# Performance work log

Hardware: AMD Instinct MI355X
Metric: run time of the kernel (lower is better)

## Reference

```python
import jax, jax.numpy as jnp
import numpy as np

B, S, H = 8, 8192, 128          # batch, num_cities, hidden_size
SSIZE, DSIZE = 2, 1             # static (x,y) feats, dynamic feats
STEPS = 20                      # station_num_lim (decode length)


def setup_inputs() -> dict:
    key = jax.random.key(0)
    ks = jax.random.split(key, 16)
    sc = 0.05
    inp = {
        'static': jax.random.normal(ks[0], (B, SSIZE, S), jnp.float32),
        'dynamic': jnp.zeros((B, DSIZE, S), jnp.float32),
        # Encoder convs (kernel_size=1 -> plain linear over channel dim)
        'W_s': jax.random.normal(ks[1], (H, SSIZE), jnp.float32) * sc,
        'b_s': jnp.zeros((H,), jnp.float32),
        'W_d': jax.random.normal(ks[2], (H, DSIZE), jnp.float32) * sc,
        'b_d': jnp.zeros((H,), jnp.float32),
        'W_dec': jax.random.normal(ks[3], (H, SSIZE), jnp.float32) * sc,
        'b_dec': jnp.zeros((H,), jnp.float32),
        # LSTMCell
        'W_ih': jax.random.normal(ks[4], (4 * H, H), jnp.float32) * sc,
        'W_hh': jax.random.normal(ks[5], (4 * H, H), jnp.float32) * sc,
        'b_ih': jnp.zeros((4 * H,), jnp.float32),
        'b_hh': jnp.zeros((4 * H,), jnp.float32),
        # Pointer projections
        'W_ref': jax.random.normal(ks[6], (H, H), jnp.float32) * sc,
        'b_ref': jnp.zeros((H,), jnp.float32),
        'W_pd': jax.random.normal(ks[7], (H, H), jnp.float32) * sc,
        'b_pd': jnp.zeros((H,), jnp.float32),
        'W_q': jax.random.normal(ks[8], (H, H), jnp.float32) * sc,
        'b_q': jnp.zeros((H,), jnp.float32),
        # Additive attention vector (Attention.W, shape (1,H) in torch)
        'W_att': jax.random.normal(ks[9], (H,), jnp.float32) * sc,
        'station_num_lim': STEPS,
    }
    return inp


def reference(static, dynamic, W_s, b_s, W_d, b_d, W_dec, b_dec,
              W_ih, W_hh, b_ih, b_hh, W_ref, b_ref, W_pd, b_pd,
              W_q, b_q, W_att, station_num_lim):
    Bb, _, Ss = static.shape
    Hh = W_s.shape[0]

    # static/dynamic encoders: Conv1d(k=1) == channelwise linear
    static_h = jnp.einsum('bis,hi->bhs', static, W_s) + b_s[None, :, None]
    dynamic_h = jnp.einsum('bis,hi->bhs', dynamic, W_d) + b_d[None, :, None]
    mask = jnp.ones((Bb, Ss), static.dtype)

    def lstm_cell(x, h, c):
        gates = x @ W_ih.T + b_ih + h @ W_hh.T + b_hh
        i, f, g, o = jnp.split(gates, 4, axis=1)
        c2 = jax.nn.sigmoid(f) * c + jax.nn.sigmoid(i) * jnp.tanh(g)
        h2 = jax.nn.sigmoid(o) * jnp.tanh(c2)
        return h2, c2

    def step(carry, _):
        dec_in, hh, cc = carry                      # dec_in: (B, SSIZE)
        dec_hidden = dec_in @ W_dec.T + b_dec       # decoder Encoder, (B, H)
        hh, cc = lstm_cell(dec_hidden, hh, cc)
        # per-step projections (as in the original Pointer.forward)
        ref = jnp.einsum('bhs,gh->bgs', static_h, W_ref) + b_ref[None, :, None]
        dyn = jnp.einsum('bhs,gh->bgs', dynamic_h, W_pd) + b_pd[None, :, None]
        q = hh @ W_q.T + b_q                        # (B, H)
        hidden = jnp.tanh(q[:, :, None] + ref + dyn)  # (B, H, S)
        attns = jnp.einsum('h,bhs->bs', W_att, hidden)
        probs = jax.nn.softmax(attns + mask * 10000.0, axis=1)
        prob = jnp.max(probs, axis=1)               # greedy (eval) select
        ptr = jnp.argmax(probs, axis=1)
        logp = jnp.log(prob)
        dec_in2 = jnp.take_along_axis(static, ptr[:, None, None], axis=2)[:, :, 0]
        return (dec_in2, hh, cc), (ptr, logp)

    dec0 = jnp.zeros((Bb, static.shape[1]), static.dtype)   # x0
    hh0 = jnp.zeros((Bb, Hh), static.dtype)
    cc0 = jnp.zeros((Bb, Hh), static.dtype)
    _, (tour_idx, tour_logp) = jax.lax.scan(
        step, (dec0, hh0, cc0), None, length=station_num_lim)
    return tour_idx.T, tour_logp.T                  # (B, steps), (B, steps)
```

## Files before the change

### kernel.cpp

```cpp
#include <hip/hip_runtime.h>
#include <hip/hip_bf16.h>


#define SS 8192
#define HH 128
#define NB 8

constexpr float kLog2e  = 1.4426950408889634f;
constexpr float kLn2    = 0.6931471805599453f;
constexpr float kBucket = 9.765625e-4f;
constexpr float kBL2e   = kLog2e * 9.765625e-4f;

__device__ __forceinline__ float fsig(float x) {
  return __builtin_amdgcn_rcpf(1.0f + __builtin_amdgcn_exp2f(-x * kLog2e));
}
__device__ __forceinline__ float ftanh(float x) {
  float z = __builtin_amdgcn_exp2f(x * (2.0f * kLog2e));
  return fmaf(-2.0f, __builtin_amdgcn_rcpf(z + 1.0f), 1.0f);
}

__device__ __forceinline__ unsigned long long cld64(const unsigned long long* p) {
  return __hip_atomic_load(p, __ATOMIC_RELAXED, __HIP_MEMORY_SCOPE_AGENT);
}
__device__ __forceinline__ void cst64(unsigned long long* p, unsigned long long v) {
  __hip_atomic_store(p, v, __ATOMIC_RELAXED, __HIP_MEMORY_SCOPE_AGENT);
}

__global__ __launch_bounds__(256, 1)
void drl4_kernel(const float* __restrict__ g_static,
                 const float* __restrict__ g_dynamic,
                 const float* __restrict__ W_s,  const float* __restrict__ b_s,
                 const float* __restrict__ W_d,  const float* __restrict__ b_d,
                 const float* __restrict__ W_dec,const float* __restrict__ b_dec,
                 const float* __restrict__ W_ih, const float* __restrict__ W_hh,
                 const float* __restrict__ b_ih, const float* __restrict__ b_hh,
                 const float* __restrict__ W_ref,const float* __restrict__ b_ref,
                 const float* __restrict__ W_pd, const float* __restrict__ b_pd,
                 const float* __restrict__ W_q,  const float* __restrict__ b_q,
                 const float* __restrict__ W_att,const int* __restrict__ steps_p,
                 float* __restrict__ out,
                 unsigned long long* __restrict__ krec,
                 unsigned long long* __restrict__ hhrec,
                 unsigned long long* __restrict__ frec) {
  const int tid = threadIdx.x;
  const int bid = blockIdx.x;
  const int b   = bid >> 5;
  const int blk = bid & 31;
  const int steps = *steps_p;

  __shared__ float4 s_pack[128];
  __shared__ float  s_ebias[128];
  __shared__ float  s_gb[512];
  __shared__ float  s_g1x[512];
  __shared__ float  s_g1y[512];
  __shared__ float  s_h[128];
  __shared__ __align__(16) float s_qe[128];
  __shared__ float  s_scr[256];

  const int city = blk * 256 + tid;
  const float sx = g_static[(b * 2 + 0) * SS + city];
  const float sy = g_static[(b * 2 + 1) * SS + city];
  const float dd = g_dynamic[b * SS + city];

  const int qrow  = (tid >> 6) * 32 + (tid & 31);
  const int qhalf = (tid >> 5) & 1;
  float wq[64];
  {
    const float* p = W_q + qrow * HH + qhalf * 64;
    #pragma unroll
    for (int j = 0; j < 64; j += 4) {
      float4 v = *(const float4*)(p + j);
      wq[j] = v.x; wq[j+1] = v.y; wq[j+2] = v.z; wq[j+3] = v.w;
    }
  }
  const int ho = tid & 15, hk = tid >> 4;
  float whh[8];
  {
    const float* p = W_hh + (blk * 16 + ho) * HH + hk * 8;
    #pragma unroll
    for (int j = 0; j < 8; j += 4) {
      float4 v = *(const float4*)(p + j);
      whh[j] = v.x; whh[j+1] = v.y; whh[j+2] = v.z; whh[j+3] = v.w;
    }
  }

  for (int g = tid; g < 512; g += 256) {
    const float* wr = W_ih + g * HH;
    float acc = b_ih[g] + b_hh[g];
    float ax = 0.f, ay = 0.f;
    for (int k = 0; k < HH; k += 4) {
      float4 w  = *(const float4*)(wr + k);
      float4 bd = *(const float4*)(b_dec + k);
      float4 d0 = *(const float4*)(W_dec + 2 * k);
      float4 d1 = *(const float4*)(W_dec + 2 * k + 4);
      acc = fmaf(w.x, bd.x, acc); ax = fmaf(w.x, d0.x, ax); ay = fmaf(w.x, d0.y, ay);
      acc = fmaf(w.y, bd.y, acc); ax = fmaf(w.y, d0.z, ax); ay = fmaf(w.y, d0.w, ay);
      acc = fmaf(w.z, bd.z, acc); ax = fmaf(w.z, d1.x, ax); ay = fmaf(w.z, d1.y, ay);
      acc = fmaf(w.w, bd.w, acc); ax = fmaf(w.w, d1.z, ax); ay = fmaf(w.w, d1.w, ay);
    }
    s_gb[g] = acc; s_g1x[g] = ax; s_g1y[g] = ay;
  }
  if (tid < 128) {
    float a0 = 0.f, a1 = 0.f, c0 = 0.f, e1 = 0.f, e2 = 0.f;
    const float* wr = W_ref + tid * HH;
    const float* wp = W_pd  + tid * HH;
    for (int k = 0; k < HH; k += 4) {
      float4 w  = *(const float4*)(wr + k);
      float4 v  = *(const float4*)(wp + k);
      float4 s0 = *(const float4*)(W_s + 2 * k);
      float4 s1 = *(const float4*)(W_s + 2 * k + 4);
      float4 bs = *(const float4*)(b_s + k);
      float4 wd = *(const float4*)(W_d + k);
      float4 bd = *(const float4*)(b_d + k);
      a0 = fmaf(w.x, s0.x, a0); a1 = fmaf(w.x, s0.y, a1); e1 = fmaf(w.x, bs.x, e1);
      c0 = fmaf(v.x, wd.x, c0); e2 = fmaf(v.x, bd.x, e2);
      a0 = fmaf(w.y, s0.z, a0); a1 = fmaf(w.y, s0.w, a1); e1 = fmaf(w.y, bs.y, e1);
      c0 = fmaf(v.y, wd.y, c0); e2 = fmaf(v.y, bd.y, e2);
      a0 = fmaf(w.z, s1.x, a0); a1 = fmaf(w.z, s1.y, a1); e1 = fmaf(w.z, bs.z, e1);
      c0 = fmaf(v.z, wd.z, c0); e2 = fmaf(v.z, bd.z, e2);
      a0 = fmaf(w.w, s1.z, a0); a1 = fmaf(w.w, s1.w, a1); e1 = fmaf(w.w, bs.w, e1);
      c0 = fmaf(v.w, wd.w, c0); e2 = fmaf(v.w, bd.w, e2);
    }
    const float sc = 2.0f * kLog2e;
    s_pack[tid]  = make_float4(a0 * sc, a1 * sc, c0 * sc, W_att[tid]);
    s_ebias[tid] = e1 + e2 + b_ref[tid] + b_pd[tid] + b_q[tid];
  }
  float cstate = 0.0f;
  __syncthreads();

  float zb[128], watt[128];
  #pragma unroll
  for (int h = 0; h < 128; ++h) {
    float4 p = s_pack[h];
    zb[h]   = __builtin_amdgcn_exp2f(fmaf(p.x, sx, fmaf(p.y, sy, p.z * dd)));
    watt[h] = p.w;
  }

  const int wv = tid >> 6;
  const int ln = tid & 63;
  for (int t = 0; t < steps; ++t) {
    float hp0 = 0.f, hp1 = 0.f, hp2 = 0.f, hp3 = 0.f;
    float selx = 0.f, sely = 0.f;
    if (t > 0) {
      if (tid < 128) {
        const unsigned expect = (unsigned)t;
        const unsigned long long* kp =
            krec + ((t - 1) & 1) * 1024 + b * 128;
        const unsigned long long* hp = hhrec + (t & 1) * 4096 + b * 512 + tid;
        unsigned long long k0, k1, h0, h1, h2, h3;
        for (;;) {
          k0 = cld64(kp + ln);       k1 = cld64(kp + 64 + ln);
          h0 = cld64(hp);            h1 = cld64(hp + 128);
          h2 = cld64(hp + 256);      h3 = cld64(hp + 384);
          if ((unsigned)(k0 >> 32) == expect && (unsigned)(k1 >> 32) == expect &&
              (unsigned)(h0 >> 32) == expect && (unsigned)(h1 >> 32) == expect &&
              (unsigned)(h2 >> 32) == expect && (unsigned)(h3 >> 32) == expect)
            break;
          __builtin_amdgcn_s_sleep(1);
        }
        unsigned u0 = (unsigned)k0, u1 = (unsigned)k1;
        unsigned wmax = u0 > u1 ? u0 : u1;
        #pragma unroll
        for (int k = 1; k < 64; k <<= 1) {
          unsigned o = __shfl_xor(wmax, k);
          wmax = wmax > o ? wmax : o;
        }
        const int ix = 8191 - (int)(wmax & 0x1FFFu);
        hp0 = __uint_as_float((unsigned)h0);
        hp1 = __uint_as_float((unsigned)h1);
        hp2 = __uint_as_float((unsigned)h2);
        hp3 = __uint_as_float((unsigned)h3);
        selx = g_static[(b * 2 + 0) * SS + ix];
        sely = g_static[(b * 2 + 1) * SS + ix];
      }
    }
    if (tid < 128) {
      float gi, gf, gg, go;
      if (t == 0) {
        gi = s_gb[tid];       gf = s_gb[tid + 128];
        gg = s_gb[tid + 256]; go = s_gb[tid + 384];
      } else {
        gi = fmaf(selx, s_g1x[tid],     fmaf(sely, s_g1y[tid],     s_gb[tid]     + hp0));
        gf = fmaf(selx, s_g1x[tid+128], fmaf(sely, s_g1y[tid+128], s_gb[tid+128] + hp1));
        gg = fmaf(selx, s_g1x[tid+256], fmaf(sely, s_g1y[tid+256], s_gb[tid+256] + hp2));
        go = fmaf(selx, s_g1x[tid+384], fmaf(sely, s_g1y[tid+384], s_gb[tid+384] + hp3));
      }
      cstate  = fmaf(fsig(gf), cstate, fsig(gi) * ftanh(gg));
      s_h[tid] = fsig(go) * ftanh(cstate);
    }
    __syncthreads();
    {
      const float* hs = s_h + (qhalf << 6);
      float qa = 0.f;
      #pragma unroll
      for (int u = 0; u < 64; ++u) qa = fmaf(wq[u], hs[u], qa);
      float qo = __shfl_xor(qa, 32);
      if (qhalf == 0) {
        float qe = (qa + qo + s_ebias[qrow]) * (2.0f * kLog2e);
        s_qe[qrow] = __builtin_amdgcn_exp2f(qe);
      }
    }
    {
      const float* hs2 = s_h + hk * 8;
      float pa = 0.f;
      #pragma unroll
      for (int u = 0; u < 8; ++u) pa = fmaf(whh[u], hs2[u], pa);
      s_scr[tid] = pa;
    }
    __syncthreads();
    if (tid < 16) {
      float acc = 0.f;
      #pragma unroll
      for (int j = 0; j < 16; ++j) acc += s_scr[j * 16 + tid];
      cst64(hhrec + ((t + 1) & 1) * 4096 + b * 512 + blk * 16 + tid,
            ((unsigned long long)(unsigned)(t + 1) << 32) |
                __float_as_uint(acc));
    }
    float a0 = 0.f, a1 = 0.f, a2 = 0.f, a3 = 0.f;
    #pragma unroll
    for (int h = 0; h < 128; h += 4) {
      float4 zq = *(const float4*)(s_qe + h);
      float z0 = zb[h+0] * zq.x, z1 = zb[h+1] * zq.y;
      float z2 = zb[h+2] * zq.z, z3 = zb[h+3] * zq.w;
      float r0 = __builtin_amdgcn_rcpf(z0 + 1.0f);
      float r1 = __builtin_amdgcn_rcpf(z1 + 1.0f);
      float r2 = __builtin_amdgcn_rcpf(z2 + 1.0f);
      float r3 = __builtin_amdgcn_rcpf(z3 + 1.0f);
      a0 = fmaf(watt[h+0], fmaf(-2.0f, r0, 1.0f), a0);
      a1 = fmaf(watt[h+1], fmaf(-2.0f, r1, 1.0f), a1);
      a2 = fmaf(watt[h+2], fmaf(-2.0f, r2, 1.0f), a2);
      a3 = fmaf(watt[h+3], fmaf(-2.0f, r3, 1.0f), a3);
    }
    float aq = ((a0 + a1) + (a2 + a3)) + 10000.0f;
    int kk = (int)((aq - 10000.0f) * 1024.0f);
    kk = kk < -8192 ? -8192 : (kk > 8191 ? 8191 : kk);
    unsigned key = ((unsigned)(kk + 8192) << 13) | (unsigned)(8191 - city);
    unsigned wmax = key;
    #pragma unroll
    for (int k = 1; k < 64; k <<= 1) {
      unsigned o = __shfl_xor(wmax, k);
      wmax = wmax > o ? wmax : o;
    }
    if (ln == 0)
      cst64(krec + (t & 1) * 1024 + b * 128 + blk * 4 + wv,
            ((unsigned long long)(unsigned)(t + 1) << 32) | wmax);
    float m_w = fmaf((float)((int)((wmax >> 13) & 0x3FFFu) - 8192), kBucket,
                     10000.0f);
    float ee = __builtin_amdgcn_exp2f((aq - m_w) * kLog2e);
    #pragma unroll
    for (int k = 1; k < 64; k <<= 1) ee += __shfl_xor(ee, k);
    if (ln == 0)
      cst64(frec + (t * 8 + b) * 128 + blk * 4 + wv,
            ((unsigned long long)__float_as_uint(ee) << 32) |
                ((unsigned)(t + 1) << 27) | wmax);
  }
  if (blk == 0) {
    for (int s = wv; s < steps; s += 4) {
      const unsigned long long* wp = frec + (s * 8 + b) * 128;
      const unsigned expect = (unsigned)(s + 1);
      unsigned long long r0, r1;
      for (;;) {
        r0 = cld64(wp + ln); r1 = cld64(wp + 64 + ln);
        if (((unsigned)r0 >> 27) == expect && ((unsigned)r1 >> 27) == expect)
          break;
        __builtin_amdgcn_s_sleep(1);
      }
      unsigned k0 = (unsigned)r0 & 0x07FFFFFFu;
      unsigned k1 = (unsigned)r1 & 0x07FFFFFFu;
      unsigned wmax = k0 > k1 ? k0 : k1;
      #pragma unroll
      for (int k = 1; k < 64; k <<= 1) {
        unsigned o = __shfl_xor(wmax, k);
        wmax = wmax > o ? wmax : o;
      }
      int K  = (int)((wmax >> 13) & 0x3FFFu) - 8192;
      int i0 = (int)((k0 >> 13) & 0x3FFFu) - 8192;
      int i1 = (int)((k1 >> 13) & 0x3FFFu) - 8192;
      float e0 = __uint_as_float((unsigned)(r0 >> 32));
      float e1 = __uint_as_float((unsigned)(r1 >> 32));
      float term = fmaf(e0, __builtin_amdgcn_exp2f((float)(i0 - K) * kBL2e),
                        e1 * __builtin_amdgcn_exp2f((float)(i1 - K) * kBL2e));
      #pragma unroll
      for (int k = 1; k < 64; k <<= 1) term += __shfl_xor(term, k);
      if (ln == 0) {
        out[b * steps + s] = (float)(8191 - (int)(wmax & 0x1FFFu));
        out[NB * steps + b * steps + s] =
            -__builtin_amdgcn_logf(term) * kLn2;
      }
    }
  }
}

extern "C" void kernel_launch(void* const* d_in, const int* in_sizes, int n_in,
                              void* d_out, int out_size, void* d_ws, size_t ws_size,
                              hipStream_t stream) {
  char* ws = (char*)d_ws;
  unsigned long long* krec  = (unsigned long long*)(ws);
  unsigned long long* hhrec = (unsigned long long*)(ws + 16384);
  unsigned long long* frec  = (unsigned long long*)(ws + 81920);
  drl4_kernel<<<dim3(256), dim3(256), 0, stream>>>(
      (const float*)d_in[0],  (const float*)d_in[1],
      (const float*)d_in[2],  (const float*)d_in[3],
      (const float*)d_in[4],  (const float*)d_in[5],
      (const float*)d_in[6],  (const float*)d_in[7],
      (const float*)d_in[8],  (const float*)d_in[9],
      (const float*)d_in[10], (const float*)d_in[11],
      (const float*)d_in[12], (const float*)d_in[13],
      (const float*)d_in[14], (const float*)d_in[15],
      (const float*)d_in[16], (const float*)d_in[17],
      (const float*)d_in[18], (const int*)d_in[19],
      (float*)d_out, krec, hhrec, frec);
}
```

Before: 209.3 us.

## Pipeline spin-wait polling, gather selected city coords before reduction, reset flags in-kernel

The inter-block spin-wait now alternates two sets of in-flight atomic loads without sleeping, so a fresh poll is always outstanding while the previous one is checked. Each lane also gathers the static coordinates of its own candidate before the wave max-reduction, then picks the winner's values with ballot and shuffle. This takes the dependent global load off the critical path after the reduction. The sync records are zeroed at kernel start and the workspace layout is reordered. The in-kernel zeroing has no grid-wide barrier before other blocks may read the records, and the tight polling raises memory traffic.

```diff
diff --git a/kernel.cpp b/kernel.cpp
--- a/kernel.cpp
+++ b/kernel.cpp
@@ -40,8 +40,8 @@
                  const float* __restrict__ W_att,const int* __restrict__ steps_p,
                  float* __restrict__ out,
                  unsigned long long* __restrict__ krec,
-                 unsigned long long* __restrict__ hhrec,
-                 unsigned long long* __restrict__ frec) {
+                 unsigned long long* __restrict__ frec,
+                 unsigned long long* __restrict__ hhrec) {
   const int tid = threadIdx.x;
   const int bid = blockIdx.x;
   const int b   = bid >> 5;
@@ -62,6 +62,9 @@
   const float sy = g_static[(b * 2 + 1) * SS + city];
   const float dd = g_dynamic[b * SS + city];
 
+  const int wv = tid >> 6;
+  const int ln = tid & 63;
+
   const int qrow  = (tid >> 6) * 32 + (tid & 31);
   const int qhalf = (tid >> 5) & 1;
   float wq[64];
@@ -82,6 +85,17 @@
       float4 v = *(const float4*)(p + j);
       whh[j] = v.x; whh[j+1] = v.y; whh[j+2] = v.z; whh[j+3] = v.w;
     }
+  }
+
+  if (ln == 0) {
+    cst64(krec + 0 * 1024 + b * 128 + blk * 4 + wv, 0ull);
+    cst64(krec + 1 * 1024 + b * 128 + blk * 4 + wv, 0ull);
+    for (int s = 0; s < steps; ++s)
+      cst64(frec + (s * 8 + b) * 128 + blk * 4 + wv, 0ull);
+  }
+  if (tid < 16) {
+    cst64(hhrec + 0 * 4096 + b * 512 + blk * 16 + tid, 0ull);
+    cst64(hhrec + 1 * 4096 + b * 512 + blk * 16 + tid, 0ull);
   }
 
   for (int g = tid; g < 512; g += 256) {
@@ -136,8 +150,6 @@
     watt[h] = p.w;
   }
 
-  const int wv = tid >> 6;
-  const int ln = tid & 63;
   for (int t = 0; t < steps; ++t) {
     float hp0 = 0.f, hp1 = 0.f, hp2 = 0.f, hp3 = 0.f;
     float selx = 0.f, sely = 0.f;
@@ -145,33 +157,58 @@
       if (tid < 128) {
         const unsigned expect = (unsigned)t;
         const unsigned long long* kp =
-            krec + ((t - 1) & 1) * 1024 + b * 128;
+            krec + ((t - 1) & 1) * 1024 + b * 128 + ln;
         const unsigned long long* hp = hhrec + (t & 1) * 4096 + b * 512 + tid;
-        unsigned long long k0, k1, h0, h1, h2, h3;
-        for (;;) {
-          k0 = cld64(kp + ln);       k1 = cld64(kp + 64 + ln);
-          h0 = cld64(hp);            h1 = cld64(hp + 128);
-          h2 = cld64(hp + 256);      h3 = cld64(hp + 384);
-          if ((unsigned)(k0 >> 32) == expect && (unsigned)(k1 >> 32) == expect &&
-              (unsigned)(h0 >> 32) == expect && (unsigned)(h1 >> 32) == expect &&
-              (unsigned)(h2 >> 32) == expect && (unsigned)(h3 >> 32) == expect)
-            break;
-          __builtin_amdgcn_s_sleep(1);
+        unsigned long long kv0, kv1, h0, h1, h2, h3;
+        {
+          unsigned long long aj, ak, a0, a1, a2, a3;
+          unsigned long long bj, bk, b0, b1, b2, b3;
+          aj = cld64(kp);       ak = cld64(kp + 64);
+          a0 = cld64(hp);       a1 = cld64(hp + 128);
+          a2 = cld64(hp + 256); a3 = cld64(hp + 384);
+          for (;;) {
+            asm volatile("" ::: "memory");
+            bj = cld64(kp);       bk = cld64(kp + 64);
+            b0 = cld64(hp);       b1 = cld64(hp + 128);
+            b2 = cld64(hp + 256); b3 = cld64(hp + 384);
+            asm volatile("" ::: "memory");
+            if ((unsigned)(aj >> 32) == expect && (unsigned)(ak >> 32) == expect &&
+                (unsigned)(a0 >> 32) == expect && (unsigned)(a1 >> 32) == expect &&
+                (unsigned)(a2 >> 32) == expect && (unsigned)(a3 >> 32) == expect) {
+              kv0 = aj; kv1 = ak; h0 = a0; h1 = a1; h2 = a2; h3 = a3; break;
+            }
+            asm volatile("" ::: "memory");
+            aj = cld64(kp);       ak = cld64(kp + 64);
+            a0 = cld64(hp);       a1 = cld64(hp + 128);
+            a2 = cld64(hp + 256); a3 = cld64(hp + 384);
+            asm volatile("" ::: "memory");
+            if ((unsigned)(bj >> 32) == expect && (unsigned)(bk >> 32) == expect &&
+                (unsigned)(b0 >> 32) == expect && (unsigned)(b1 >> 32) == expect &&
+                (unsigned)(b2 >> 32) == expect && (unsigned)(b3 >> 32) == expect) {
+              kv0 = bj; kv1 = bk; h0 = b0; h1 = b1; h2 = b2; h3 = b3; break;
+            }
+          }
         }
-        unsigned u0 = (unsigned)k0, u1 = (unsigned)k1;
-        unsigned wmax = u0 > u1 ? u0 : u1;
+        unsigned u0 = (unsigned)kv0, u1 = (unsigned)kv1;
+        const unsigned myk = u0 > u1 ? u0 : u1;
+        const int my_ix = 8191 - (int)(myk & 0x1FFFu);
+        const float* gsb = g_static + (b * 2) * SS;
+        float cx = gsb[my_ix];
+        float cy = gsb[SS + my_ix];
+        unsigned wmax = myk;
         #pragma unroll
         for (int k = 1; k < 64; k <<= 1) {
           unsigned o = __shfl_xor(wmax, k);
           wmax = wmax > o ? wmax : o;
         }
-        const int ix = 8191 - (int)(wmax & 0x1FFFu);
+        unsigned long long win = __ballot(myk == wmax);
+        int src = __ffsll(win) - 1;
+        selx = __shfl(cx, src);
+        sely = __shfl(cy, src);
         hp0 = __uint_as_float((unsigned)h0);
         hp1 = __uint_as_float((unsigned)h1);
         hp2 = __uint_as_float((unsigned)h2);
         hp3 = __uint_as_float((unsigned)h3);
-        selx = g_static[(b * 2 + 0) * SS + ix];
-        sely = g_static[(b * 2 + 1) * SS + ix];
       }
     }
     if (tid < 128) {
@@ -294,10 +331,9 @@
 extern "C" void kernel_launch(void* const* d_in, const int* in_sizes, int n_in,
                               void* d_out, int out_size, void* d_ws, size_t ws_size,
                               hipStream_t stream) {
-  char* ws = (char*)d_ws;
-  unsigned long long* krec  = (unsigned long long*)(ws);
-  unsigned long long* hhrec = (unsigned long long*)(ws + 16384);
-  unsigned long long* frec  = (unsigned long long*)(ws + 81920);
+  unsigned long long* krec  = (unsigned long long*)d_ws;
+  unsigned long long* frec  = (unsigned long long*)((char*)d_ws + 16384);
+  unsigned long long* hhrec = (unsigned long long*)((char*)d_ws + 180224);
   drl4_kernel<<<dim3(256), dim3(256), 0, stream>>>(
       (const float*)d_in[0],  (const float*)d_in[1],
       (const float*)d_in[2],  (const float*)d_in[3],
@@ -309,5 +345,5 @@
       (const float*)d_in[14], (const float*)d_in[15],
       (const float*)d_in[16], (const float*)d_in[17],
       (const float*)d_in[18], (const int*)d_in[19],
-      (float*)d_out, krec, hhrec, frec);
-}
+      (float*)d_out, krec, frec, hhrec);
+}
```

Measured after the change: 212.8 us. No clear change (+1.6%).
